# Performance work log

Hardware: AMD Instinct MI355X
Metric: run time of the kernel (lower is better)

Reference implementation:

```python
import jax, jax.numpy as jnp
import numpy as np

B, D, F, H = 256, 9, 8, 256   # batch of trees, tree depth, input features, hidden
N = 2 ** (D + 1) - 1          # total nodes per full binary tree (heap layout)


def _init(key, shape, fan_in):
    return jax.random.normal(key, shape, jnp.float32) * (1.0 / np.sqrt(fan_in))


def setup_inputs() -> dict:
    key = jax.random.key(0)
    ks = jax.random.split(key, 6)
    return {
        "data": jax.random.normal(ks[0], (B, N, F), jnp.float32),
        "Wu": _init(ks[1], (H, F), F),
        "bu": jnp.zeros((H,), jnp.float32),
        "Wr": _init(ks[2], (3 * H, 3 * H), 3 * H),
        "br": jnp.zeros((3 * H,), jnp.float32),
        "Wh": _init(ks[3], (H, 3 * H), 3 * H),
        "bh": jnp.zeros((H,), jnp.float32),
        "Wz": _init(ks[4], (4 * H, 4 * H), 4 * H),
        "bz": jnp.zeros((4 * H,), jnp.float32),
        "Wp": _init(ks[5], (1, H), H),
        "bp": jnp.zeros((1,), jnp.float32),
    }


def reference(data, Wu, bu, Wr, br, Wh, bh, Wz, bz, Wp, bp):
    # data: [B, N, F] node features in heap (level-order) layout;
    # children of the i-th node of level l are nodes 2i, 2i+1 of level l+1.
    b, n_nodes, _ = data.shape
    L = (n_nodes + 1) // 2          # number of leaves
    depth = L.bit_length() - 1
    h_dim = Wu.shape[0]

    # leaf embedding u for every node (leaf() is applied at every tree node)
    u = jnp.einsum('bnf,hf->bnh', data, Wu) + bu          # [B, N, H]
    h = u[:, L - 1:, :]                                    # leaf level states [B, L, H]

    for l in range(depth - 1, -1, -1):                     # bottom-up over levels
        n = 2 ** l
        parent = u[:, n - 1:2 * n - 1, :]                  # [B, n, H]
        h_l, h_r = h[:, 0::2, :], h[:, 1::2, :]            # [B, n, H] each
        hhu = jnp.concatenate([parent, h_l, h_r], axis=-1)  # [B, n, 3H]
        r = jax.nn.sigmoid(jnp.einsum('bnk,jk->bnj', hhu, Wr) + br)
        h_new = jax.nn.relu(jnp.einsum('bnk,hk->bnh', r * hhu, Wh) + bh)
        hhhu = jnp.concatenate([h_new, hhu], axis=-1)      # [B, n, 4H]
        zlin = jnp.einsum('bnk,jk->bnj', hhhu, Wz) + bz    # [B, n, 4H]
        z = jax.nn.softmax(zlin.reshape(b, n, 4, h_dim), axis=2)
        h = (z * hhhu.reshape(b, n, 4, h_dim)).sum(axis=2)  # gated combine -> [B, n, H]

    # h is [B, 1, H] at the root; logits head
    logits = jnp.einsum('bnh,oh->bno', h, Wp) + bp          # [B, 1, 1]
    return logits[:, 0, 0]                                  # [B]
```

## Files before the change

### kernel.cpp

```cpp
#include <hip/hip_runtime.h>
#include <math.h>

#define BB 256
#define NN 1023
#define FF 8
#define HH 256
#define DEPTH 9

enum { EPI_NONE = 0, EPI_SIGMUL = 1, EPI_RELU = 2, EPI_COMBINE = 3 };

typedef __bf16 bf16x8_t __attribute__((ext_vector_type(8)));
typedef float f32x4_t __attribute__((ext_vector_type(4)));

__device__ __forceinline__ void stage16(const void* g, void* l) {
    __builtin_amdgcn_global_load_lds(
        (const __attribute__((address_space(1))) void*)g,
        (__attribute__((address_space(3))) void*)l,
        16, 0, 0);
}

__device__ __forceinline__ int xcd_remap(int hw, int nwg) {
    const int xcd = hw & 7, k0 = hw >> 3;
    const int qq = nwg >> 3, rr = nwg & 7;
    return (xcd < rr ? xcd * (qq + 1) : rr * (qq + 1) + (xcd - rr) * qq) + k0;
}

template <int EPI>
__global__ __launch_bounds__(1024, 4) void gemm256w(
    const __bf16* __restrict__ A, int lda,
    const __bf16* __restrict__ W,
    const float* __restrict__ bias,
    const __bf16* __restrict__ aux, int ldaux,
    void* __restrict__ Cout, int ldc,
    int r0c,
    int K)
{
    __shared__ __bf16 lds[2][2][256 * 64];
    const int tid = threadIdx.x;
    const int lane = tid & 63;
    const int w = tid >> 6;
    const int wr = w >> 2, wc = w & 3;

    const int nwg = gridDim.x * gridDim.y;
    const int hw = blockIdx.y * gridDim.x + blockIdx.x;
    const int wg = xcd_remap(hw, nwg);
    const int bm0 = (wg / gridDim.x) * 256;
    const int bn0 = (wg % gridDim.x) * 256;

    const int srow = tid >> 3;
    const int scolz = ((tid & 7) ^ (srow & 7)) * 8;

    f32x4_t acc[4][4];
#pragma unroll
    for (int i = 0; i < 4; ++i)
#pragma unroll
        for (int j = 0; j < 4; ++j) acc[i][j] = (f32x4_t){0.f, 0.f, 0.f, 0.f};

    const int rA = lane & 15;
    const int klane = (lane >> 4) * 8;
    const int rxor = (lane & 7) * 8;
    const int NT = K >> 6;

#define STAGE_T(t, buf)                                                        \
    do {                                                                       \
        const int kk_ = (t) << 6;                                              \
        stage16(A + (size_t)(bm0 + srow) * lda + kk_ + scolz,                  \
                &lds[buf][0][w * 512]);                                        \
        stage16(A + (size_t)(bm0 + 128 + srow) * lda + kk_ + scolz,            \
                &lds[buf][0][8192 + w * 512]);                                 \
        stage16(W + (size_t)(bn0 + srow) * K + kk_ + scolz,                    \
                &lds[buf][1][w * 512]);                                        \
        stage16(W + (size_t)(bn0 + 128 + srow) * K + kk_ + scolz,              \
                &lds[buf][1][8192 + w * 512]);                                 \
    } while (0)
#define LDA_F(As_, i, ks) \
    (*(const bf16x8_t*)&(As_)[(wr * 64 + (i) * 16 + rA) * 64 + (((ks) * 32 + klane) ^ rxor)])
#define LDB_F(Bs_, j, ks) \
    (*(const bf16x8_t*)&(Bs_)[(wc * 64 + (j) * 16 + rA) * 64 + (((ks) * 32 + klane) ^ rxor)])

    STAGE_T(0, 0);
    STAGE_T(1, 1);
    asm volatile("s_waitcnt vmcnt(4)" ::: "memory");
    __builtin_amdgcn_s_barrier();

    for (int t = 0; t < NT; ++t) {
        const int cur = t & 1;
        const __bf16* As = lds[cur][0];
        const __bf16* Bs = lds[cur][1];
        bf16x8_t af[4], bf[4];

#pragma unroll
        for (int j = 0; j < 4; ++j) bf[j] = LDB_F(Bs, j, 0);
#pragma unroll
        for (int i = 0; i < 4; ++i) af[i] = LDA_F(As, i, 0);
#pragma unroll
        for (int i = 0; i < 4; ++i)
#pragma unroll
            for (int j = 0; j < 4; ++j)
                acc[i][j] = __builtin_amdgcn_mfma_f32_16x16x32_bf16(
                    af[i], bf[j], acc[i][j], 0, 0, 0);
#pragma unroll
        for (int j = 0; j < 4; ++j) bf[j] = LDB_F(Bs, j, 1);
#pragma unroll
        for (int i = 0; i < 4; ++i) af[i] = LDA_F(As, i, 1);
#pragma unroll
        for (int i = 0; i < 2; ++i)
#pragma unroll
            for (int j = 0; j < 4; ++j)
                acc[i][j] = __builtin_amdgcn_mfma_f32_16x16x32_bf16(
                    af[i], bf[j], acc[i][j], 0, 0, 0);

        asm volatile("s_waitcnt lgkmcnt(0)" ::: "memory");
        __builtin_amdgcn_s_barrier();
        if (t + 2 < NT) STAGE_T(t + 2, cur);

        __builtin_amdgcn_s_setprio(1);
#pragma unroll
        for (int i = 2; i < 4; ++i)
#pragma unroll
            for (int j = 0; j < 4; ++j)
                acc[i][j] = __builtin_amdgcn_mfma_f32_16x16x32_bf16(
                    af[i], bf[j], acc[i][j], 0, 0, 0);
        __builtin_amdgcn_s_setprio(0);

        if (t + 1 < NT) {
            if (t + 2 < NT) {
                asm volatile("s_waitcnt vmcnt(4)" ::: "memory");
            } else {
                asm volatile("s_waitcnt vmcnt(0)" ::: "memory");
            }
            __builtin_amdgcn_s_barrier();
        }
    }
#undef STAGE_T
#undef LDA_F
#undef LDB_F

    const int hi = lane >> 4;
    const int r = lane & 15;

    if (EPI == EPI_COMBINE) {
        __bf16* pan = &lds[0][0][0];
        const int g0 = bn0 >> 2;
        float bz4[4];
#pragma unroll
        for (int g = 0; g < 4; ++g) bz4[g] = bias[bn0 + wc * 64 + g * 16 + r];
        const int G = g0 + wc * 16 + r;
#pragma unroll
        for (int i = 0; i < 4; ++i) {
#pragma unroll
            for (int reg = 0; reg < 4; ++reg) {
                const int lr = wr * 64 + i * 16 + hi * 4 + reg;
                const int gr = bm0 + lr;
                float z0 = acc[i][0][reg] + bz4[0];
                float z1 = acc[i][1][reg] + bz4[1];
                float z2 = acc[i][2][reg] + bz4[2];
                float z3 = acc[i][3][reg] + bz4[3];
                float mx = fmaxf(fmaxf(z0, z1), fmaxf(z2, z3));
                float e0 = __expf(z0 - mx), e1 = __expf(z1 - mx);
                float e2 = __expf(z2 - mx), e3 = __expf(z3 - mx);
                const __bf16* hrow = aux + (size_t)gr * ldaux + G;
                float hv = (e0 * (float)hrow[0] + e1 * (float)hrow[256] +
                            e2 * (float)hrow[512] + e3 * (float)hrow[768]) /
                           (e0 + e1 + e2 + e3);
                pan[lr * 72 + wc * 16 + r] = (__bf16)hv;
            }
        }
        __syncthreads();
        const int cbase = r0c + bm0;
#pragma unroll
        for (int it = 0; it < 2; ++it) {
            const int unit = it * 1024 + tid;
            const int row = unit >> 3;
            const int c8 = (unit & 7) * 8;
            const int crow = cbase + row;
            bf16x8_t vv = *(const bf16x8_t*)&pan[row * 72 + c8];
            *(bf16x8_t*)((__bf16*)Cout + (size_t)(crow >> 1) * 1024 + 512 +
                         (crow & 1) * 256 + g0 + c8) = vv;
        }
    } else if (EPI == EPI_SIGMUL) {
        __bf16* pan = &lds[0][0][0];
        float bv[4];
#pragma unroll
        for (int j = 0; j < 4; ++j) bv[j] = bias[bn0 + wc * 64 + j * 16 + r];
#pragma unroll
        for (int j = 0; j < 4; ++j) {
            const int lc = wc * 64 + j * 16 + r;
            const int gc = bn0 + lc;
#pragma unroll
            for (int i = 0; i < 4; ++i) {
#pragma unroll
                for (int reg = 0; reg < 4; ++reg) {
                    const int lr = wr * 64 + i * 16 + hi * 4 + reg;
                    const int gr = bm0 + lr;
                    float v = acc[i][j][reg] + bv[j];
                    float s = 1.0f / (1.0f + __expf(-v));
                    v = s * (float)aux[(size_t)gr * ldaux + gc];
                    pan[lr * 256 + lc] = (__bf16)v;
                }
            }
        }
        __syncthreads();
#pragma unroll
        for (int it = 0; it < 8; ++it) {
            const int unit = it * 1024 + tid;
            const int row = unit >> 5;
            const int c8 = (unit & 31) * 8;
            bf16x8_t vv = *(const bf16x8_t*)&pan[row * 256 + c8];
            *(bf16x8_t*)((__bf16*)Cout + (size_t)(bm0 + row) * ldc + bn0 + c8) = vv;
        }
    } else {
#pragma unroll
        for (int j = 0; j < 4; ++j) {
            const int gc = bn0 + wc * 64 + j * 16 + r;
            const float bv = bias[gc];
#pragma unroll
            for (int i = 0; i < 4; ++i) {
#pragma unroll
                for (int reg = 0; reg < 4; ++reg) {
                    const int gr = bm0 + wr * 64 + i * 16 + hi * 4 + reg;
                    float v = acc[i][j][reg] + bv;
                    if (EPI == EPI_RELU) v = fmaxf(v, 0.0f);
                    ((__bf16*)Cout)[(size_t)gr * ldc + gc] = (__bf16)v;
                }
            }
        }
    }
}

template <int EPI>
__global__ __launch_bounds__(256) void gemm_mfma(
    const __bf16* __restrict__ A, int lda,
    const __bf16* __restrict__ W,
    const float* __restrict__ bias,
    const __bf16* __restrict__ aux, int ldaux,
    void* __restrict__ Cout, int ldc,
    int r0c, int topar,
    int K)
{
    __shared__ __bf16 As[128 * 32];
    __shared__ __bf16 Bs[128 * 32];
    const int tid = threadIdx.x;
    const int lane = tid & 63;
    const int w = tid >> 6;
    const int wr = w >> 1, wc = w & 1;

    const int nwg = gridDim.x * gridDim.y;
    const int hw = blockIdx.y * gridDim.x + blockIdx.x;
    const int wg = xcd_remap(hw, nwg);
    const int bm0 = (wg / gridDim.x) * 128;
    const int bn0 = (wg % gridDim.x) * 128;

    const int srow = lane >> 2;
    const int scol = (lane & 3) * 8;

    f32x4_t acc[4][4];
#pragma unroll
    for (int i = 0; i < 4; ++i)
#pragma unroll
        for (int j = 0; j < 4; ++j) acc[i][j] = (f32x4_t){0.f, 0.f, 0.f, 0.f};

    const int rA = lane & 15;
    const int kslot = (lane >> 4) * 8;

    for (int kk = 0; kk < K; kk += 32) {
        stage16(A + (size_t)(bm0 + w * 16 + srow) * lda + kk + scol,
                &As[(w * 16) * 32]);
        stage16(A + (size_t)(bm0 + 64 + w * 16 + srow) * lda + kk + scol,
                &As[(64 + w * 16) * 32]);
        stage16(W + (size_t)(bn0 + w * 16 + srow) * K + kk + scol,
                &Bs[(w * 16) * 32]);
        stage16(W + (size_t)(bn0 + 64 + w * 16 + srow) * K + kk + scol,
                &Bs[(64 + w * 16) * 32]);
        __syncthreads();

        bf16x8_t af[4], bfr[4];
#pragma unroll
        for (int i = 0; i < 4; ++i)
            af[i] = *(const bf16x8_t*)&As[(wr * 64 + i * 16 + rA) * 32 + kslot];
#pragma unroll
        for (int j = 0; j < 4; ++j)
            bfr[j] = *(const bf16x8_t*)&Bs[(wc * 64 + j * 16 + rA) * 32 + kslot];
#pragma unroll
        for (int i = 0; i < 4; ++i)
#pragma unroll
            for (int j = 0; j < 4; ++j)
                acc[i][j] = __builtin_amdgcn_mfma_f32_16x16x32_bf16(
                    af[i], bfr[j], acc[i][j], 0, 0, 0);
        __syncthreads();
    }

    if (EPI == EPI_COMBINE) {
        const int r = lane & 15;
        const int G = ((bn0 + wc * 64) >> 2) + r;
        float bz4[4];
#pragma unroll
        for (int g = 0; g < 4; ++g) bz4[g] = bias[bn0 + wc * 64 + g * 16 + r];
#pragma unroll
        for (int i = 0; i < 4; ++i) {
#pragma unroll
            for (int reg = 0; reg < 4; ++reg) {
                const int gr = bm0 + wr * 64 + i * 16 + (lane >> 4) * 4 + reg;
                float z0 = acc[i][0][reg] + bz4[0];
                float z1 = acc[i][1][reg] + bz4[1];
                float z2 = acc[i][2][reg] + bz4[2];
                float z3 = acc[i][3][reg] + bz4[3];
                float mx = fmaxf(fmaxf(z0, z1), fmaxf(z2, z3));
                float e0 = __expf(z0 - mx), e1 = __expf(z1 - mx);
                float e2 = __expf(z2 - mx), e3 = __expf(z3 - mx);
                const __bf16* hrow = aux + (size_t)gr * ldaux + G;
                float hv = (e0 * (float)hrow[0] + e1 * (float)hrow[256] +
                            e2 * (float)hrow[512] + e3 * (float)hrow[768]) /
                           (e0 + e1 + e2 + e3);
                if (topar) {
                    const int crow = r0c + gr;
                    ((__bf16*)Cout)[(size_t)(crow >> 1) * 1024 + 512 +
                                    (crow & 1) * 256 + G] = (__bf16)hv;
                } else {
                    ((__bf16*)Cout)[(size_t)gr * ldc + G] = (__bf16)hv;
                }
            }
        }
    } else {
#pragma unroll
        for (int j = 0; j < 4; ++j) {
            const int gc = bn0 + wc * 64 + j * 16 + (lane & 15);
            const float bv = bias[gc];
#pragma unroll
            for (int i = 0; i < 4; ++i) {
#pragma unroll
                for (int reg = 0; reg < 4; ++reg) {
                    const int gr = bm0 + wr * 64 + i * 16 + (lane >> 4) * 4 + reg;
                    float v = acc[i][j][reg] + bv;
                    if (EPI == EPI_SIGMUL) {
                        float s = 1.0f / (1.0f + __expf(-v));
                        v = s * (float)aux[(size_t)gr * ldaux + gc];
                        ((__bf16*)Cout)[(size_t)gr * ldc + gc] = (__bf16)v;
                    } else if (EPI == EPI_RELU) {
                        v = fmaxf(v, 0.0f);
                        ((__bf16*)Cout)[(size_t)gr * ldc + gc] = (__bf16)v;
                    } else {
                        ((float*)Cout)[(size_t)gr * ldc + gc] = v;
                    }
                }
            }
        }
    }
}

__global__ __launch_bounds__(256) void convert_weights(
    const float* __restrict__ Wr, const float* __restrict__ Wh,
    const float* __restrict__ Wz, const float* __restrict__ bz,
    __bf16* __restrict__ Wrb, __bf16* __restrict__ Whb,
    __bf16* __restrict__ Wzb, float* __restrict__ bzp)
{
    const int NR = 768 * 768, NH2 = 256 * 768, NZ = 1024 * 1024;
    const int idx0 = blockIdx.x * 256 + threadIdx.x;
    for (int i = idx0; i < NR + NH2 + NZ; i += gridDim.x * 256) {
        if (i < NR) Wrb[i] = (__bf16)Wr[i];
        else if (i < NR + NH2) Whb[i - NR] = (__bf16)Wh[i - NR];
        else {
            const int z = i - NR - NH2;
            const int p = z >> 10, k = z & 1023;
            const int o = ((p >> 4) & 3) * 256 + (p >> 6) * 16 + (p & 15);
            Wzb[z] = (__bf16)Wz[(size_t)o * 1024 + k];
        }
    }
    if (idx0 < 1024) {
        const int p = idx0;
        const int o = ((p >> 4) & 3) * 256 + (p >> 6) * 16 + (p & 15);
        bzp[p] = bz[o];
    }
}

__global__ __launch_bounds__(256) void build_leaf(
    const float* __restrict__ data, const float* __restrict__ Wu,
    const float* __restrict__ bu, __bf16* __restrict__ slice, int r0)
{
    const int blk = xcd_remap(blockIdx.x, gridDim.x);
    const int row = blk * 8 + (threadIdx.x >> 5);
    const int c0 = (threadIdx.x & 31) * 8;
    const int i = r0 + row;
    const int b = i >> 8;
    const int m = i & 255;

    float wv[8][8];
#pragma unroll
    for (int cc = 0; cc < 8; ++cc) {
        float4 w0 = *(const float4*)&Wu[(c0 + cc) * 8];
        float4 w1 = *(const float4*)&Wu[(c0 + cc) * 8 + 4];
        wv[cc][0] = w0.x; wv[cc][1] = w0.y; wv[cc][2] = w0.z; wv[cc][3] = w0.w;
        wv[cc][4] = w1.x; wv[cc][5] = w1.y; wv[cc][6] = w1.z; wv[cc][7] = w1.w;
    }
    float buv[8];
#pragma unroll
    for (int cc = 0; cc < 8; ++cc) buv[cc] = bu[c0 + cc];

    __bf16* rowp = slice + (size_t)row * 1024;
    {
        const float* dp = data + ((size_t)b * NN + 255 + m) * FF;
        float4 d0 = *(const float4*)dp, d1 = *(const float4*)(dp + 4);
        float dv[8] = {d0.x, d0.y, d0.z, d0.w, d1.x, d1.y, d1.z, d1.w};
        bf16x8_t o;
#pragma unroll
        for (int cc = 0; cc < 8; ++cc) {
            float acc = buv[cc];
#pragma unroll
            for (int f = 0; f < 8; ++f) acc += dv[f] * wv[cc][f];
            o[cc] = (__bf16)acc;
        }
        *(bf16x8_t*)&rowp[256 + c0] = o;
    }
    const float* dl = data + ((size_t)b * NN + 511 + 2 * m) * FF;
#pragma unroll
    for (int side = 0; side < 2; ++side) {
        const float* dp = dl + side * FF;
        float4 d0 = *(const float4*)dp, d1 = *(const float4*)(dp + 4);
        float dv[8] = {d0.x, d0.y, d0.z, d0.w, d1.x, d1.y, d1.z, d1.w};
        bf16x8_t o;
#pragma unroll
        for (int cc = 0; cc < 8; ++cc) {
            float acc = buv[cc];
#pragma unroll
            for (int f = 0; f < 8; ++f) acc += dv[f] * wv[cc][f];
            o[cc] = (__bf16)acc;
        }
        *(bf16x8_t*)&rowp[512 + side * 256 + c0] = o;
    }
}

__global__ __launch_bounds__(256) void build_u(
    const float* __restrict__ data, const float* __restrict__ Wu,
    const float* __restrict__ bu, __bf16* __restrict__ slice, int l, int r0)
{
    const int n = 1 << l;
    const int blk = xcd_remap(blockIdx.x, gridDim.x);
    const int row = blk * 8 + (threadIdx.x >> 5);
    const int c0 = (threadIdx.x & 31) * 8;
    const int i = r0 + row;
    const int b = i >> l;
    const int m = i & (n - 1);

    float wv[8][8];
#pragma unroll
    for (int cc = 0; cc < 8; ++cc) {
        float4 w0 = *(const float4*)&Wu[(c0 + cc) * 8];
        float4 w1 = *(const float4*)&Wu[(c0 + cc) * 8 + 4];
        wv[cc][0] = w0.x; wv[cc][1] = w0.y; wv[cc][2] = w0.z; wv[cc][3] = w0.w;
        wv[cc][4] = w1.x; wv[cc][5] = w1.y; wv[cc][6] = w1.z; wv[cc][7] = w1.w;
    }
    const float* dp = data + ((size_t)b * NN + (n - 1) + m) * FF;
    float4 d0 = *(const float4*)dp, d1 = *(const float4*)(dp + 4);
    float dv[8] = {d0.x, d0.y, d0.z, d0.w, d1.x, d1.y, d1.z, d1.w};
    bf16x8_t o;
#pragma unroll
    for (int cc = 0; cc < 8; ++cc) {
        float acc = bu[c0 + cc];
#pragma unroll
        for (int f = 0; f < 8; ++f) acc += dv[f] * wv[cc][f];
        o[cc] = (__bf16)acc;
    }
    *(bf16x8_t*)&slice[(size_t)row * 1024 + 256 + c0] = o;
}

__global__ __launch_bounds__(256) void final_kernel(
    const __bf16* __restrict__ hfin, const float* __restrict__ Wp,
    const float* __restrict__ bp, float* __restrict__ out)
{
    const int b = blockIdx.x;
    const int t = threadIdx.x;
    __shared__ float red[256];
    red[t] = (float)hfin[(size_t)b * HH + t] * Wp[t];
    __syncthreads();
    for (int s = 128; s > 0; s >>= 1) {
        if (t < s) red[t] += red[t + s];
        __syncthreads();
    }
    if (t == 0) out[b] = red[0] + bp[0];
}

extern "C" void kernel_launch(void* const* d_in, const int* in_sizes, int n_in,
                              void* d_out, int out_size, void* d_ws, size_t ws_size,
                              hipStream_t stream)
{
    const float* data = (const float*)d_in[0];
    const float* Wu = (const float*)d_in[1];
    const float* bu = (const float*)d_in[2];
    const float* Wr = (const float*)d_in[3];
    const float* br = (const float*)d_in[4];
    const float* Wh = (const float*)d_in[5];
    const float* bh = (const float*)d_in[6];
    const float* Wz = (const float*)d_in[7];
    const float* bz = (const float*)d_in[8];
    const float* Wp = (const float*)d_in[9];
    const float* bp = (const float*)d_in[10];
    float* out = (float*)d_out;

    const size_t CAP = 16384;
    char* w = (char*)d_ws;
    __bf16* hhhuA = (__bf16*)w; w += (size_t)65536 * 1024 * 2;
    __bf16* hhhuB = (__bf16*)w; w += (size_t)32768 * 1024 * 2;
    __bf16* rh = (__bf16*)w;    w += CAP * 768 * 2;
    __bf16* hRoot = (__bf16*)w; w += (size_t)256 * 256 * 2;
    __bf16* Wrb = (__bf16*)w;   w += (size_t)768 * 768 * 2;
    __bf16* Whb = (__bf16*)w;   w += (size_t)256 * 768 * 2;
    __bf16* Wzb = (__bf16*)w;   w += (size_t)1024 * 1024 * 2;
    float* bzp = (float*)w;     w += 1024 * 4;

    convert_weights<<<2048, 256, 0, stream>>>(Wr, Wh, Wz, bz, Wrb, Whb, Wzb, bzp);

    for (int l = DEPTH - 1; l >= 0; --l) {
        const size_t M = (size_t)BB << l;
        __bf16* cur = (l & 1) ? hhhuB : hhhuA;
        __bf16* par = (l == 0) ? hRoot : ((l & 1) ? hhhuA : hhhuB);
        const int topar = (l > 0);
        for (size_t r0 = 0; r0 < M; r0 += CAP) {
            const int R = (int)((M - r0 < CAP) ? (M - r0) : CAP);
            __bf16* slice = cur + (size_t)r0 * 1024;
            if (l == 8)
                build_leaf<<<R / 8, 256, 0, stream>>>(data, Wu, bu, slice, (int)r0);
            else
                build_u<<<R / 8, 256, 0, stream>>>(data, Wu, bu, slice, l, (int)r0);
            if (R >= 16384) {
                gemm256w<EPI_SIGMUL><<<dim3(3, R / 256), 1024, 0, stream>>>(
                    slice + 256, 1024, Wrb, br, slice + 256, 1024, rh, 768, 0, 768);
            } else {
                gemm_mfma<EPI_SIGMUL><<<dim3(6, R / 128), 256, 0, stream>>>(
                    slice + 256, 1024, Wrb, br, slice + 256, 1024, rh, 768, 0, 0, 768);
            }
            gemm_mfma<EPI_RELU><<<dim3(2, R / 128), 256, 0, stream>>>(
                rh, 768, Whb, bh, nullptr, 0, slice, 1024, 0, 0, 768);
            if (R >= 16384) {
                gemm256w<EPI_COMBINE><<<dim3(4, R / 256), 1024, 0, stream>>>(
                    slice, 1024, Wzb, bzp, slice, 1024, par, HH, (int)r0, 1024);
            } else {
                gemm_mfma<EPI_COMBINE><<<dim3(8, R / 128), 256, 0, stream>>>(
                    slice, 1024, Wzb, bzp, slice, 1024, par, HH, (int)r0, topar, 1024);
            }
        }
    }
    final_kernel<<<BB, 256, 0, stream>>>(hRoot, Wp, bp, out);
}
```

Measured before the change: 1.176 ms.

## Fold leaf embedding Wu into Wr and Wz to shrink GEMM K dimension

The parent's u=Wu·x+bu term is algebraically folded into the Wr and Wz weights, so the GEMMs read the raw 8 input features (padded to 64) instead of the 256-wide embedding. This cuts K from 768 to 576 for the reset GEMM and from 1024 to 832 for the gate GEMM, and shrinks the per-row workspace stride. The embedding u is still built into a separate buffer for the elementwise gating and combine epilogues. The costs are extra fold kernels, an extra u buffer read in the epilogues, and bf16 rounding of the folded weights.

```diff
diff --git a/kernel.cpp b/kernel.cpp
--- a/kernel.cpp
+++ b/kernel.cpp
@@ -6,8 +6,9 @@
 #define FF 8
 #define HH 256
 #define DEPTH 9
-
-enum { EPI_NONE = 0, EPI_SIGMUL = 1, EPI_RELU = 2, EPI_COMBINE = 3 };
+#define LDW 832
+
+enum { EPI_SIGMUL = 1, EPI_RELU = 2, EPI_COMBINE = 3 };
 
 typedef __bf16 bf16x8_t __attribute__((ext_vector_type(8)));
 typedef float f32x4_t __attribute__((ext_vector_type(4)));
@@ -30,10 +31,10 @@
     const __bf16* __restrict__ A, int lda,
     const __bf16* __restrict__ W,
     const float* __restrict__ bias,
-    const __bf16* __restrict__ aux, int ldaux,
+    const __bf16* __restrict__ slice,
+    const __bf16* __restrict__ ubuf,
     void* __restrict__ Cout, int ldc,
-    int r0c,
-    int K)
+    int r0c, int K)
 {
     __shared__ __bf16 lds[2][2][256 * 64];
     const int tid = threadIdx.x;
@@ -159,9 +160,12 @@
                 float mx = fmaxf(fmaxf(z0, z1), fmaxf(z2, z3));
                 float e0 = __expf(z0 - mx), e1 = __expf(z1 - mx);
                 float e2 = __expf(z2 - mx), e3 = __expf(z3 - mx);
-                const __bf16* hrow = aux + (size_t)gr * ldaux + G;
-                float hv = (e0 * (float)hrow[0] + e1 * (float)hrow[256] +
-                            e2 * (float)hrow[512] + e3 * (float)hrow[768]) /
+                const __bf16* srow_ = slice + (size_t)gr * LDW;
+                float a0v = (float)srow_[G];
+                float a1v = (float)ubuf[(size_t)gr * HH + G];
+                float a2v = (float)srow_[320 + G];
+                float a3v = (float)srow_[576 + G];
+                float hv = (e0 * a0v + e1 * a1v + e2 * a2v + e3 * a3v) /
                            (e0 + e1 + e2 + e3);
                 pan[lr * 72 + wc * 16 + r] = (__bf16)hv;
             }
@@ -175,10 +179,10 @@
             const int c8 = (unit & 7) * 8;
             const int crow = cbase + row;
             bf16x8_t vv = *(const bf16x8_t*)&pan[row * 72 + c8];
-            *(bf16x8_t*)((__bf16*)Cout + (size_t)(crow >> 1) * 1024 + 512 +
+            *(bf16x8_t*)((__bf16*)Cout + (size_t)(crow >> 1) * LDW + 320 +
                          (crow & 1) * 256 + g0 + c8) = vv;
         }
-    } else if (EPI == EPI_SIGMUL) {
+    } else {
         __bf16* pan = &lds[0][0][0];
         float bv[4];
 #pragma unroll
@@ -195,8 +199,10 @@
                     const int gr = bm0 + lr;
                     float v = acc[i][j][reg] + bv[j];
                     float s = 1.0f / (1.0f + __expf(-v));
-                    v = s * (float)aux[(size_t)gr * ldaux + gc];
-                    pan[lr * 256 + lc] = (__bf16)v;
+                    float a = (gc < 256)
+                                  ? (float)ubuf[(size_t)gr * HH + gc]
+                                  : (float)slice[(size_t)gr * LDW + 64 + gc];
+                    pan[lr * 256 + lc] = (__bf16)(s * a);
                 }
             }
         }
@@ -209,22 +215,6 @@
             bf16x8_t vv = *(const bf16x8_t*)&pan[row * 256 + c8];
             *(bf16x8_t*)((__bf16*)Cout + (size_t)(bm0 + row) * ldc + bn0 + c8) = vv;
         }
-    } else {
-#pragma unroll
-        for (int j = 0; j < 4; ++j) {
-            const int gc = bn0 + wc * 64 + j * 16 + r;
-            const float bv = bias[gc];
-#pragma unroll
-            for (int i = 0; i < 4; ++i) {
-#pragma unroll
-                for (int reg = 0; reg < 4; ++reg) {
-                    const int gr = bm0 + wr * 64 + i * 16 + hi * 4 + reg;
-                    float v = acc[i][j][reg] + bv;
-                    if (EPI == EPI_RELU) v = fmaxf(v, 0.0f);
-                    ((__bf16*)Cout)[(size_t)gr * ldc + gc] = (__bf16)v;
-                }
-            }
-        }
     }
 }
 
@@ -233,10 +223,10 @@
     const __bf16* __restrict__ A, int lda,
     const __bf16* __restrict__ W,
     const float* __restrict__ bias,
-    const __bf16* __restrict__ aux, int ldaux,
+    const __bf16* __restrict__ slice,
+    const __bf16* __restrict__ ubuf,
     void* __restrict__ Cout, int ldc,
-    int r0c, int topar,
-    int K)
+    int r0c, int topar, int K)
 {
     __shared__ __bf16 As[128 * 32];
     __shared__ __bf16 Bs[128 * 32];
@@ -290,8 +280,8 @@
         __syncthreads();
     }
 
+    const int r = lane & 15;
     if (EPI == EPI_COMBINE) {
-        const int r = lane & 15;
         const int G = ((bn0 + wc * 64) >> 2) + r;
         float bz4[4];
 #pragma unroll
@@ -308,13 +298,15 @@
                 float mx = fmaxf(fmaxf(z0, z1), fmaxf(z2, z3));
                 float e0 = __expf(z0 - mx), e1 = __expf(z1 - mx);
                 float e2 = __expf(z2 - mx), e3 = __expf(z3 - mx);
-                const __bf16* hrow = aux + (size_t)gr * ldaux + G;
-                float hv = (e0 * (float)hrow[0] + e1 * (float)hrow[256] +
-                            e2 * (float)hrow[512] + e3 * (float)hrow[768]) /
+                const __bf16* srow_ = slice + (size_t)gr * LDW;
+                float hv = (e0 * (float)srow_[G] +
+                            e1 * (float)ubuf[(size_t)gr * HH + G] +
+                            e2 * (float)srow_[320 + G] +
+                            e3 * (float)srow_[576 + G]) /
                            (e0 + e1 + e2 + e3);
                 if (topar) {
                     const int crow = r0c + gr;
-                    ((__bf16*)Cout)[(size_t)(crow >> 1) * 1024 + 512 +
+                    ((__bf16*)Cout)[(size_t)(crow >> 1) * LDW + 320 +
                                     (crow & 1) * 256 + G] = (__bf16)hv;
                 } else {
                     ((__bf16*)Cout)[(size_t)gr * ldc + G] = (__bf16)hv;
@@ -324,7 +316,7 @@
     } else {
 #pragma unroll
         for (int j = 0; j < 4; ++j) {
-            const int gc = bn0 + wc * 64 + j * 16 + (lane & 15);
+            const int gc = bn0 + wc * 64 + j * 16 + r;
             const float bv = bias[gc];
 #pragma unroll
             for (int i = 0; i < 4; ++i) {
@@ -334,13 +326,13 @@
                     float v = acc[i][j][reg] + bv;
                     if (EPI == EPI_SIGMUL) {
                         float s = 1.0f / (1.0f + __expf(-v));
-                        v = s * (float)aux[(size_t)gr * ldaux + gc];
-                        ((__bf16*)Cout)[(size_t)gr * ldc + gc] = (__bf16)v;
-                    } else if (EPI == EPI_RELU) {
+                        float a = (gc < 256)
+                                      ? (float)ubuf[(size_t)gr * HH + gc]
+                                      : (float)slice[(size_t)gr * LDW + 64 + gc];
+                        ((__bf16*)Cout)[(size_t)gr * ldc + gc] = (__bf16)(s * a);
+                    } else {
                         v = fmaxf(v, 0.0f);
                         ((__bf16*)Cout)[(size_t)gr * ldc + gc] = (__bf16)v;
-                    } else {
-                        ((float*)Cout)[(size_t)gr * ldc + gc] = v;
                     }
                 }
             }
@@ -348,38 +340,75 @@
     }
 }
 
-__global__ __launch_bounds__(256) void convert_weights(
-    const float* __restrict__ Wr, const float* __restrict__ Wh,
-    const float* __restrict__ Wz, const float* __restrict__ bz,
-    __bf16* __restrict__ Wrb, __bf16* __restrict__ Whb,
-    __bf16* __restrict__ Wzb, float* __restrict__ bzp)
-{
-    const int NR = 768 * 768, NH2 = 256 * 768, NZ = 1024 * 1024;
-    const int idx0 = blockIdx.x * 256 + threadIdx.x;
-    for (int i = idx0; i < NR + NH2 + NZ; i += gridDim.x * 256) {
-        if (i < NR) Wrb[i] = (__bf16)Wr[i];
-        else if (i < NR + NH2) Whb[i - NR] = (__bf16)Wh[i - NR];
-        else {
-            const int z = i - NR - NH2;
-            const int p = z >> 10, k = z & 1023;
-            const int o = ((p >> 4) & 3) * 256 + (p >> 6) * 16 + (p & 15);
-            Wzb[z] = (__bf16)Wz[(size_t)o * 1024 + k];
-        }
-    }
-    if (idx0 < 1024) {
-        const int p = idx0;
-        const int o = ((p >> 4) & 3) * 256 + (p >> 6) * 16 + (p & 15);
-        bzp[p] = bz[o];
-    }
+__global__ __launch_bounds__(256) void convert_wh(
+    const float* __restrict__ Wh, __bf16* __restrict__ Whb)
+{
+    const int NH2 = 256 * 768;
+    for (int i = blockIdx.x * 256 + threadIdx.x; i < NH2; i += gridDim.x * 256)
+        Whb[i] = (__bf16)Wh[i];
+}
+
+__global__ __launch_bounds__(256) void fold_wr(
+    const float* __restrict__ Wr, const float* __restrict__ Wu,
+    const float* __restrict__ bu, const float* __restrict__ br,
+    __bf16* __restrict__ Wrp, float* __restrict__ brp)
+{
+    const int j = blockIdx.x;
+    const int c = threadIdx.x;
+    __shared__ float red[256];
+    const float wjc = Wr[(size_t)j * 768 + c];
+    red[c] = wjc * bu[c];
+    __syncthreads();
+    for (int s = 128; s > 0; s >>= 1) { if (c < s) red[c] += red[c + s]; __syncthreads(); }
+    if (c == 0) brp[j] = br[j] + red[0];
+    for (int f = 0; f < 8; ++f) {
+        __syncthreads();
+        red[c] = wjc * Wu[c * 8 + f];
+        __syncthreads();
+        for (int s = 128; s > 0; s >>= 1) { if (c < s) red[c] += red[c + s]; __syncthreads(); }
+        if (c == 0) Wrp[(size_t)j * 576 + f] = (__bf16)red[0];
+    }
+    if (c >= 8 && c < 64) Wrp[(size_t)j * 576 + c] = (__bf16)0.0f;
+    Wrp[(size_t)j * 576 + 64 + c]  = (__bf16)Wr[(size_t)j * 768 + 256 + c];
+    Wrp[(size_t)j * 576 + 320 + c] = (__bf16)Wr[(size_t)j * 768 + 512 + c];
+}
+
+__global__ __launch_bounds__(256) void fold_wz(
+    const float* __restrict__ Wz, const float* __restrict__ Wu,
+    const float* __restrict__ bu, const float* __restrict__ bz,
+    __bf16* __restrict__ Wzp, float* __restrict__ bzpf)
+{
+    const int p = blockIdx.x;
+    const int c = threadIdx.x;
+    const int o = ((p >> 4) & 3) * 256 + (p >> 6) * 16 + (p & 15);
+    __shared__ float red[256];
+    const float wuc = Wz[(size_t)o * 1024 + 256 + c];
+    red[c] = wuc * bu[c];
+    __syncthreads();
+    for (int s = 128; s > 0; s >>= 1) { if (c < s) red[c] += red[c + s]; __syncthreads(); }
+    if (c == 0) bzpf[p] = bz[o] + red[0];
+    for (int f = 0; f < 8; ++f) {
+        __syncthreads();
+        red[c] = wuc * Wu[c * 8 + f];
+        __syncthreads();
+        for (int s = 128; s > 0; s >>= 1) { if (c < s) red[c] += red[c + s]; __syncthreads(); }
+        if (c == 0) Wzp[(size_t)p * 832 + 256 + f] = (__bf16)red[0];
+    }
+    if (c >= 8 && c < 64) Wzp[(size_t)p * 832 + 256 + c] = (__bf16)0.0f;
+    Wzp[(size_t)p * 832 + c]       = (__bf16)Wz[(size_t)o * 1024 + c];
+    Wzp[(size_t)p * 832 + 320 + c] = (__bf16)Wz[(size_t)o * 1024 + 512 + c];
+    Wzp[(size_t)p * 832 + 576 + c] = (__bf16)Wz[(size_t)o * 1024 + 768 + c];
 }
 
 __global__ __launch_bounds__(256) void build_leaf(
     const float* __restrict__ data, const float* __restrict__ Wu,
-    const float* __restrict__ bu, __bf16* __restrict__ slice, int r0)
+    const float* __restrict__ bu, __bf16* __restrict__ slice,
+    __bf16* __restrict__ ubuf, int r0)
 {
     const int blk = xcd_remap(blockIdx.x, gridDim.x);
     const int row = blk * 8 + (threadIdx.x >> 5);
-    const int c0 = (threadIdx.x & 31) * 8;
+    const int lc = threadIdx.x & 31;
+    const int c0 = lc * 8;
     const int i = r0 + row;
     const int b = i >> 8;
     const int m = i & 255;
@@ -396,10 +425,10 @@
 #pragma unroll
     for (int cc = 0; cc < 8; ++cc) buv[cc] = bu[c0 + cc];
 
-    __bf16* rowp = slice + (size_t)row * 1024;
+    __bf16* rowp = slice + (size_t)row * LDW;
+    const float* dpar = data + ((size_t)b * NN + 255 + m) * FF;
     {
-        const float* dp = data + ((size_t)b * NN + 255 + m) * FF;
-        float4 d0 = *(const float4*)dp, d1 = *(const float4*)(dp + 4);
+        float4 d0 = *(const float4*)dpar, d1 = *(const float4*)(dpar + 4);
         float dv[8] = {d0.x, d0.y, d0.z, d0.w, d1.x, d1.y, d1.z, d1.w};
         bf16x8_t o;
 #pragma unroll
@@ -409,7 +438,14 @@
             for (int f = 0; f < 8; ++f) acc += dv[f] * wv[cc][f];
             o[cc] = (__bf16)acc;
         }
-        *(bf16x8_t*)&rowp[256 + c0] = o;
+        *(bf16x8_t*)&ubuf[(size_t)row * HH + c0] = o;
+        if (lc < 8) {
+            bf16x8_t dp;
+#pragma unroll
+            for (int cc = 0; cc < 8; ++cc)
+                dp[cc] = (lc == 0) ? (__bf16)dv[cc] : (__bf16)0.0f;
+            *(bf16x8_t*)&rowp[256 + lc * 8] = dp;
+        }
     }
     const float* dl = data + ((size_t)b * NN + 511 + 2 * m) * FF;
 #pragma unroll
@@ -425,18 +461,20 @@
             for (int f = 0; f < 8; ++f) acc += dv[f] * wv[cc][f];
             o[cc] = (__bf16)acc;
         }
-        *(bf16x8_t*)&rowp[512 + side * 256 + c0] = o;
+        *(bf16x8_t*)&rowp[320 + side * 256 + c0] = o;
     }
 }
 
 __global__ __launch_bounds__(256) void build_u(
     const float* __restrict__ data, const float* __restrict__ Wu,
-    const float* __restrict__ bu, __bf16* __restrict__ slice, int l, int r0)
+    const float* __restrict__ bu, __bf16* __restrict__ slice,
+    __bf16* __restrict__ ubuf, int l, int r0)
 {
     const int n = 1 << l;
     const int blk = xcd_remap(blockIdx.x, gridDim.x);
     const int row = blk * 8 + (threadIdx.x >> 5);
-    const int c0 = (threadIdx.x & 31) * 8;
+    const int lc = threadIdx.x & 31;
+    const int c0 = lc * 8;
     const int i = r0 + row;
     const int b = i >> l;
     const int m = i & (n - 1);
@@ -460,7 +498,14 @@
         for (int f = 0; f < 8; ++f) acc += dv[f] * wv[cc][f];
         o[cc] = (__bf16)acc;
     }
-    *(bf16x8_t*)&slice[(size_t)row * 1024 + 256 + c0] = o;
+    *(bf16x8_t*)&ubuf[(size_t)row * HH + c0] = o;
+    if (lc < 8) {
+        bf16x8_t dpd;
+#pragma unroll
+        for (int cc = 0; cc < 8; ++cc)
+            dpd[cc] = (lc == 0) ? (__bf16)dv[cc] : (__bf16)0.0f;
+        *(bf16x8_t*)&slice[(size_t)row * LDW + 256 + lc * 8] = dpd;
+    }
 }
 
 __global__ __launch_bounds__(256) void final_kernel(
@@ -498,16 +543,20 @@
 
     const size_t CAP = 16384;
     char* w = (char*)d_ws;
-    __bf16* hhhuA = (__bf16*)w; w += (size_t)65536 * 1024 * 2;
-    __bf16* hhhuB = (__bf16*)w; w += (size_t)32768 * 1024 * 2;
+    __bf16* hhhuA = (__bf16*)w; w += (size_t)65536 * LDW * 2;
+    __bf16* hhhuB = (__bf16*)w; w += (size_t)32768 * LDW * 2;
     __bf16* rh = (__bf16*)w;    w += CAP * 768 * 2;
+    __bf16* ubuf = (__bf16*)w;  w += CAP * HH * 2;
     __bf16* hRoot = (__bf16*)w; w += (size_t)256 * 256 * 2;
-    __bf16* Wrb = (__bf16*)w;   w += (size_t)768 * 768 * 2;
     __bf16* Whb = (__bf16*)w;   w += (size_t)256 * 768 * 2;
-    __bf16* Wzb = (__bf16*)w;   w += (size_t)1024 * 1024 * 2;
-    float* bzp = (float*)w;     w += 1024 * 4;
-
-    convert_weights<<<2048, 256, 0, stream>>>(Wr, Wh, Wz, bz, Wrb, Whb, Wzb, bzp);
+    __bf16* Wrp = (__bf16*)w;   w += (size_t)768 * 576 * 2;
+    float* brp = (float*)w;     w += 768 * 4;
+    __bf16* Wzp = (__bf16*)w;   w += (size_t)1024 * 832 * 2;
+    float* bzpf = (float*)w;    w += 1024 * 4;
+
+    convert_wh<<<768, 256, 0, stream>>>(Wh, Whb);
+    fold_wr<<<768, 256, 0, stream>>>(Wr, Wu, bu, br, Wrp, brp);
+    fold_wz<<<1024, 256, 0, stream>>>(Wz, Wu, bu, bz, Wzp, bzpf);
 
     for (int l = DEPTH - 1; l >= 0; --l) {
         const size_t M = (size_t)BB << l;
@@ -516,26 +565,26 @@
         const int topar = (l > 0);
         for (size_t r0 = 0; r0 < M; r0 += CAP) {
             const int R = (int)((M - r0 < CAP) ? (M - r0) : CAP);
-            __bf16* slice = cur + (size_t)r0 * 1024;
+            __bf16* slice = cur + (size_t)r0 * LDW;
             if (l == 8)
-                build_leaf<<<R / 8, 256, 0, stream>>>(data, Wu, bu, slice, (int)r0);
+                build_leaf<<<R / 8, 256, 0, stream>>>(data, Wu, bu, slice, ubuf, (int)r0);
             else
-                build_u<<<R / 8, 256, 0, stream>>>(data, Wu, bu, slice, l, (int)r0);
+                build_u<<<R / 8, 256, 0, stream>>>(data, Wu, bu, slice, ubuf, l, (int)r0);
             if (R >= 16384) {
                 gemm256w<EPI_SIGMUL><<<dim3(3, R / 256), 1024, 0, stream>>>(
-                    slice + 256, 1024, Wrb, br, slice + 256, 1024, rh, 768, 0, 768);
+                    slice + 256, LDW, Wrp, brp, slice, ubuf, rh, 768, 0, 576);
             } else {
                 gemm_mfma<EPI_SIGMUL><<<dim3(6, R / 128), 256, 0, stream>>>(
-                    slice + 256, 1024, Wrb, br, slice + 256, 1024, rh, 768, 0, 0, 768);
+                    slice + 256, LDW, Wrp, brp, slice, ubuf, rh, 768, 0, 0, 576);
             }
             gemm_mfma<EPI_RELU><<<dim3(2, R / 128), 256, 0, stream>>>(
-                rh, 768, Whb, bh, nullptr, 0, slice, 1024, 0, 0, 768);
+                rh, 768, Whb, bh, nullptr, nullptr, slice, LDW, 0, 0, 768);
             if (R >= 16384) {
                 gemm256w<EPI_COMBINE><<<dim3(4, R / 256), 1024, 0, stream>>>(
-                    slice, 1024, Wzb, bzp, slice, 1024, par, HH, (int)r0, 1024);
+                    slice, LDW, Wzp, bzpf, slice, ubuf, par, HH, (int)r0, 832);
             } else {
                 gemm_mfma<EPI_COMBINE><<<dim3(8, R / 128), 256, 0, stream>>>(
-                    slice, 1024, Wzb, bzp, slice, 1024, par, HH, (int)r0, topar, 1024);
+                    slice, LDW, Wzp, bzpf, slice, ubuf, par, HH, (int)r0, topar, 832);
             }
         }
     }
```

After: 1.213 ms. 3.1% more time.
